# Kernel optimization log

Hardware: AMD Instinct MI355X
Metric: run time of the kernel (lower is better)

The kernel has to match this reference:

```python
import jax, jax.numpy as jnp
from jax import lax
import numpy as np

B, T, D, H, K = 16, 2048, 512, 512, 2

def setup_inputs() -> dict:
    key = jax.random.key(0)
    k1, k2, k3 = jax.random.split(key, 3)
    inputs = jax.random.normal(k1, (B, T, D), dtype=jnp.float32)
    conv_w = jax.random.normal(k2, (3 * H, D, K), dtype=jnp.float32) * (1.0 / np.sqrt(D * K))
    conv_b = jax.random.normal(k3, (3 * H,), dtype=jnp.float32) * 0.01
    return {"inputs": inputs, "conv_w": conv_w, "conv_b": conv_b}

def reference(inputs, conv_w, conv_b):
    # inputs: [B, T, D]; conv_w: [3H, D, K]; causal conv via left-pad K-1
    k = conv_w.shape[-1]
    h = conv_w.shape[0] // 3
    x = jnp.transpose(inputs, (0, 2, 1))                      # [B, D, T]
    x = jnp.pad(x, ((0, 0), (0, 0), (k - 1, 0)))              # left pad
    gates = lax.conv_general_dilated(
        x, conv_w, window_strides=(1,), padding='VALID',
        dimension_numbers=('NCH', 'OIH', 'NCH'))              # [B, 3H, T]
    gates = jnp.transpose(gates, (0, 2, 1)) + conv_b          # [B, T, 3H]
    Z, F, O = jnp.split(gates, 3, axis=2)
    Z = jnp.tanh(Z)
    F = jax.nn.sigmoid(F)
    O = jax.nn.sigmoid(O)

    # fo-pool: c_t = f_t * c_{t-1} + (1 - f_t) * z_t, c_{-1} = 0
    def step(c, zf):
        z, f = zf
        c_ = f * c + (1.0 - f) * z
        return c_, c_

    c0 = jnp.zeros((Z.shape[0], h), dtype=Z.dtype)
    _, C = lax.scan(step, c0, (jnp.swapaxes(Z, 0, 1), jnp.swapaxes(F, 0, 1)))
    C = jnp.swapaxes(C, 0, 1)                                 # [B, T, H]
    return C, O * C
```

## Files before the change

kernel.cpp:

```cpp
#include <hip/hip_runtime.h>


#define MTOT 32768
#define NTOT 1536
#define KTOT 1024
#define DCH  512
#define TLEN 2048
#define NB   16

#define SC 32
#define LC 64

typedef __bf16 bf16x8 __attribute__((ext_vector_type(8)));
typedef float  f32x4  __attribute__((ext_vector_type(4)));

__device__ __forceinline__ unsigned short f2bf(float x) {
    unsigned u = __float_as_uint(x);
    u += 0x7FFFu + ((u >> 16) & 1u);
    return (unsigned short)(u >> 16);
}
__device__ __forceinline__ float sigmoidf_(float x) {
    return 1.f / (1.f + __expf(-x));
}

__global__ __launch_bounds__(256) void make_A(const float* __restrict__ in,
                                              unsigned short* __restrict__ A) {
    size_t i = (size_t)blockIdx.x * 256 + threadIdx.x;
    size_t e = i * 8;
    size_t m = e >> 10;
    int    j = (int)(e & 1023);
    alignas(16) unsigned short h[8];
    if (((m & (TLEN - 1)) == 0) && (j < DCH)) {
#pragma unroll
        for (int r = 0; r < 8; ++r) h[r] = 0;
    } else {
        const float* src = in + ((long long)m - 1) * DCH + j;
        float4 a = *(const float4*)src;
        float4 b = *(const float4*)(src + 4);
        h[0] = f2bf(a.x); h[1] = f2bf(a.y); h[2] = f2bf(a.z); h[3] = f2bf(a.w);
        h[4] = f2bf(b.x); h[5] = f2bf(b.y); h[6] = f2bf(b.z); h[7] = f2bf(b.w);
    }
    *(int4*)(A + e) = *(const int4*)h;
}

__global__ __launch_bounds__(256) void make_B(const float* __restrict__ w,
                                              unsigned short* __restrict__ Bt) {
    int i = blockIdx.x * 256 + threadIdx.x;
    int o = i >> 9, d = i & 511;
    float w0 = w[(size_t)(o * 512 + d) * 2];
    float w1 = w[(size_t)(o * 512 + d) * 2 + 1];
    Bt[(size_t)o * 1024 + d]       = f2bf(w0);
    Bt[(size_t)o * 1024 + 512 + d] = f2bf(w1);
}

__global__ __launch_bounds__(256) void gemm_gates(const unsigned short* __restrict__ A,
                                                  const unsigned short* __restrict__ B,
                                                  const float* __restrict__ bias,
                                                  unsigned short* __restrict__ GT) {
    __shared__ int4 sA[512];
    __shared__ int4 sB[512];

    const int tid = threadIdx.x;
    const int bx  = blockIdx.x;
    const int xcd = bx & 7;
    const int i2  = bx >> 3;
    const int mT  = xcd * 32 + i2 / 12;
    const int nT  = i2 % 12;
    const int m0  = mT * 128, n0 = nT * 128;

    const int mloc = tid >> 2;
    const int qsw  = (tid & 3) ^ ((mloc >> 1) & 3);
    const unsigned short* ga0 = A + (size_t)(m0 + mloc) * 1024 + qsw * 8;
    const unsigned short* ga1 = A + (size_t)(m0 + 64 + mloc) * 1024 + qsw * 8;
    const unsigned short* gb0 = B + (size_t)(n0 + mloc) * 1024 + qsw * 8;
    const unsigned short* gb1 = B + (size_t)(n0 + 64 + mloc) * 1024 + qsw * 8;

    char* la0 = (char*)sA + tid * 16;
    char* la1 = (char*)sA + 4096 + tid * 16;
    char* lb0 = (char*)sB + tid * 16;
    char* lb1 = (char*)sB + 4096 + tid * 16;

    const int lane = tid & 63;
    const int wv   = tid >> 6;
    const int wm   = (wv & 1) * 64, wn = (wv >> 1) * 64;
    const int lr   = lane & 15, lq = lane >> 4;

    int sAidx[4], sBidx[4];
#pragma unroll
    for (int i = 0; i < 4; ++i) {
        int mi = wm + 16 * i + lr;
        sAidx[i] = mi * 4 + (lq ^ ((mi >> 1) & 3));
        int ni = wn + 16 * i + lr;
        sBidx[i] = ni * 4 + (lq ^ ((ni >> 1) & 3));
    }

    f32x4 acc[4][4] = {};

    for (int kt = 0; kt < KTOT; kt += 32) {
        __builtin_amdgcn_global_load_lds(
            (__attribute__((address_space(1))) void*)(void*)ga0,
            (__attribute__((address_space(3))) void*)la0, 16, 0, 0);
        __builtin_amdgcn_global_load_lds(
            (__attribute__((address_space(1))) void*)(void*)ga1,
            (__attribute__((address_space(3))) void*)la1, 16, 0, 0);
        __builtin_amdgcn_global_load_lds(
            (__attribute__((address_space(1))) void*)(void*)gb0,
            (__attribute__((address_space(3))) void*)lb0, 16, 0, 0);
        __builtin_amdgcn_global_load_lds(
            (__attribute__((address_space(1))) void*)(void*)gb1,
            (__attribute__((address_space(3))) void*)lb1, 16, 0, 0);
        ga0 += 32; ga1 += 32; gb0 += 32; gb1 += 32;
        __syncthreads();

        bf16x8 af[4], bfr[4];
#pragma unroll
        for (int i = 0; i < 4; ++i) af[i]  = __builtin_bit_cast(bf16x8, sA[sAidx[i]]);
#pragma unroll
        for (int j = 0; j < 4; ++j) bfr[j] = __builtin_bit_cast(bf16x8, sB[sBidx[j]]);

#pragma unroll
        for (int i = 0; i < 4; ++i)
#pragma unroll
            for (int j = 0; j < 4; ++j)
                acc[i][j] = __builtin_amdgcn_mfma_f32_16x16x32_bf16(af[i], bfr[j],
                                                                    acc[i][j], 0, 0, 0);
        __syncthreads();
    }

#pragma unroll
    for (int j = 0; j < 4; ++j) {
        int gn = n0 + wn + 16 * j + lr;
        float bj = bias[gn];
#pragma unroll
        for (int i = 0; i < 4; ++i) {
            int rowb = m0 + wm + 16 * i + lq * 4;
            alignas(8) unsigned short pk[4];
#pragma unroll
            for (int r = 0; r < 4; ++r) pk[r] = f2bf(acc[i][j][r] + bj);
            *(int2*)(GT + (size_t)gn * MTOT + rowb) = *(const int2*)pk;
        }
    }
}

__global__ __launch_bounds__(256) void scan_agg(const unsigned short* __restrict__ GT,
                                                float* __restrict__ P,
                                                float* __restrict__ C) {
    int idx = blockIdx.x * 256 + threadIdx.x;
    int h = idx & 511, s = (idx >> 9) & 31, b = idx >> 14;
    const unsigned short* gz = GT + (size_t)h * MTOT + (size_t)b * TLEN + s * LC;
    const unsigned short* gf = gz + (size_t)DCH * MTOT;

    float p = 1.f, c = 0.f;
#pragma unroll 2
    for (int k = 0; k < LC; k += 8) {
        bf16x8 zv = *(const bf16x8*)(gz + k);
        bf16x8 fv = *(const bf16x8*)(gf + k);
#pragma unroll
        for (int r = 0; r < 8; ++r) {
            float f = sigmoidf_((float)fv[r]);
            float z = 2.f * sigmoidf_(2.f * (float)zv[r]) - 1.f;
            c = f * c + (1.f - f) * z;
            p *= f;
        }
    }
    P[idx] = p;
    C[idx] = c;
}

__global__ __launch_bounds__(256) void scan_chunks(const float* __restrict__ P,
                                                   const float* __restrict__ C,
                                                   float* __restrict__ I) {
    int j = blockIdx.x * 256 + threadIdx.x;
    int b = j >> 9, h = j & 511;
    size_t base = (size_t)b * (SC * DCH) + h;
    float cc = 0.f;
#pragma unroll
    for (int s = 0; s < SC; ++s) {
        size_t o = base + (size_t)s * DCH;
        I[o] = cc;
        cc = P[o] * cc + C[o];
    }
}

__global__ __launch_bounds__(256) void scan_apply(const unsigned short* __restrict__ GT,
                                                  const float* __restrict__ I,
                                                  float* __restrict__ out) {
    int idx = blockIdx.x * 256 + threadIdx.x;
    int h = idx & 511, s = (idx >> 9) & 31, b = idx >> 14;
    const unsigned short* gz = GT + (size_t)h * MTOT + (size_t)b * TLEN + s * LC;
    const unsigned short* gf = gz + (size_t)DCH * MTOT;
    const unsigned short* go = gf + (size_t)DCH * MTOT;

    const size_t BTH = (size_t)NB * TLEN * DCH;
    float* oC  = out + ((size_t)b * TLEN + s * LC) * DCH + h;
    float* oOC = oC + BTH;

    float c = I[idx];
#pragma unroll 2
    for (int k = 0; k < LC; k += 8) {
        bf16x8 zv = *(const bf16x8*)(gz + k);
        bf16x8 fv = *(const bf16x8*)(gf + k);
        bf16x8 ov = *(const bf16x8*)(go + k);
#pragma unroll
        for (int r = 0; r < 8; ++r) {
            float f = sigmoidf_((float)fv[r]);
            float z = 2.f * sigmoidf_(2.f * (float)zv[r]) - 1.f;
            float o = sigmoidf_((float)ov[r]);
            c = f * c + (1.f - f) * z;
            oC[(size_t)(k + r) * DCH]  = c;
            oOC[(size_t)(k + r) * DCH] = o * c;
        }
    }
}

extern "C" void kernel_launch(void* const* d_in, const int* in_sizes, int n_in,
                              void* d_out, int out_size, void* d_ws, size_t ws_size,
                              hipStream_t stream) {
    const float* in   = (const float*)d_in[0];
    const float* w    = (const float*)d_in[1];
    const float* bias = (const float*)d_in[2];
    float* out = (float*)d_out;

    unsigned short* Abf = (unsigned short*)d_ws;
    unsigned short* Bbf = Abf + (size_t)MTOT * 1024;
    unsigned short* GT  = Bbf + (size_t)NTOT * 1024;

    float* P = (float*)d_ws;
    float* C = P + (size_t)NB * SC * DCH;
    float* I = C + (size_t)NB * SC * DCH;

    make_A<<<dim3(16384), dim3(256), 0, stream>>>(in, Abf);
    make_B<<<dim3(3072),  dim3(256), 0, stream>>>(w, Bbf);
    gemm_gates<<<dim3(3072), dim3(256), 0, stream>>>(Abf, Bbf, bias, GT);
    scan_agg<<<dim3(1024), dim3(256), 0, stream>>>(GT, P, C);
    scan_chunks<<<dim3(32), dim3(256), 0, stream>>>(P, C, I);
    scan_apply<<<dim3(1024), dim3(256), 0, stream>>>(GT, I, out);
}
```

Baseline: 427.1 us.

## Replace im2col buffer with padded input and vectorize scan kernels

Replaces the duplicated K=2 im2col A matrix with a single left-padded bf16 copy of the input. The GEMM reads each row's 1024-wide K slice as two consecutive padded rows, which halves the conversion kernel's writes and the workspace footprint. scan_agg now issues all of its gate loads up front. scan_apply handles two channels per thread with float2 output stores and batched register loads. The trade-off is higher register pressure and half as many blocks in scan_apply.

Measured after the change: 469.3 us. 9.9% more time.

```diff
diff --git a/kernel.cpp b/kernel.cpp
--- a/kernel.cpp
+++ b/kernel.cpp
@@ -23,24 +23,26 @@
     return 1.f / (1.f + __expf(-x));
 }
 
-__global__ __launch_bounds__(256) void make_A(const float* __restrict__ in,
-                                              unsigned short* __restrict__ A) {
-    size_t i = (size_t)blockIdx.x * 256 + threadIdx.x;
-    size_t e = i * 8;
-    size_t m = e >> 10;
-    int    j = (int)(e & 1023);
-    alignas(16) unsigned short h[8];
-    if (((m & (TLEN - 1)) == 0) && (j < DCH)) {
-#pragma unroll
-        for (int r = 0; r < 8; ++r) h[r] = 0;
+__global__ __launch_bounds__(256) void make_X(const float* __restrict__ in,
+                                              unsigned short* __restrict__ X) {
+    int rloc = threadIdx.x >> 6;
+    int c8   = (threadIdx.x & 63) << 3;
+    int row  = blockIdx.x * 4 + rloc;
+    int b    = blockIdx.y;
+    if (row >= 2049) return;
+    unsigned short* dst = X + ((size_t)b * 2049 + row) * 512 + c8;
+    alignas(16) unsigned short hh[8];
+    if (row == 0) {
+#pragma unroll
+        for (int r = 0; r < 8; ++r) hh[r] = 0;
     } else {
-        const float* src = in + ((long long)m - 1) * DCH + j;
+        const float* src = in + ((size_t)b * 2048 + row - 1) * 512 + c8;
         float4 a = *(const float4*)src;
-        float4 b = *(const float4*)(src + 4);
-        h[0] = f2bf(a.x); h[1] = f2bf(a.y); h[2] = f2bf(a.z); h[3] = f2bf(a.w);
-        h[4] = f2bf(b.x); h[5] = f2bf(b.y); h[6] = f2bf(b.z); h[7] = f2bf(b.w);
-    }
-    *(int4*)(A + e) = *(const int4*)h;
+        float4 v = *(const float4*)(src + 4);
+        hh[0] = f2bf(a.x); hh[1] = f2bf(a.y); hh[2] = f2bf(a.z); hh[3] = f2bf(a.w);
+        hh[4] = f2bf(v.x); hh[5] = f2bf(v.y); hh[6] = f2bf(v.z); hh[7] = f2bf(v.w);
+    }
+    *(int4*)dst = *(const int4*)hh;
 }
 
 __global__ __launch_bounds__(256) void make_B(const float* __restrict__ w,
@@ -53,7 +55,7 @@
     Bt[(size_t)o * 1024 + 512 + d] = f2bf(w1);
 }
 
-__global__ __launch_bounds__(256) void gemm_gates(const unsigned short* __restrict__ A,
+__global__ __launch_bounds__(256) void gemm_gates(const unsigned short* __restrict__ X,
                                                   const unsigned short* __restrict__ B,
                                                   const float* __restrict__ bias,
                                                   unsigned short* __restrict__ GT) {
@@ -67,11 +69,14 @@
     const int mT  = xcd * 32 + i2 / 12;
     const int nT  = i2 % 12;
     const int m0  = mT * 128, n0 = nT * 128;
+    const int b0  = m0 >> 11;
+    const int t0  = m0 & 2047;
 
     const int mloc = tid >> 2;
     const int qsw  = (tid & 3) ^ ((mloc >> 1) & 3);
-    const unsigned short* ga0 = A + (size_t)(m0 + mloc) * 1024 + qsw * 8;
-    const unsigned short* ga1 = A + (size_t)(m0 + 64 + mloc) * 1024 + qsw * 8;
+    const unsigned short* ga0 =
+        X + ((size_t)b0 * 2049 + t0 + mloc) * 512 + qsw * 8;
+    const unsigned short* ga1 = ga0 + (size_t)64 * 512;
     const unsigned short* gb0 = B + (size_t)(n0 + mloc) * 1024 + qsw * 8;
     const unsigned short* gb1 = B + (size_t)(n0 + 64 + mloc) * 1024 + qsw * 8;
 
@@ -147,14 +152,20 @@
                                                 float* __restrict__ C) {
     int idx = blockIdx.x * 256 + threadIdx.x;
     int h = idx & 511, s = (idx >> 9) & 31, b = idx >> 14;
-    const unsigned short* gz = GT + (size_t)h * MTOT + (size_t)b * TLEN + s * LC;
+    const unsigned short* gz = GT + (size_t)h * MTOT + (size_t)b * TLEN + (size_t)s * LC;
     const unsigned short* gf = gz + (size_t)DCH * MTOT;
 
+    int4 rz[8], rf[8];
+#pragma unroll
+    for (int q = 0; q < 8; ++q) rz[q] = *(const int4*)(gz + 8 * q);
+#pragma unroll
+    for (int q = 0; q < 8; ++q) rf[q] = *(const int4*)(gf + 8 * q);
+
     float p = 1.f, c = 0.f;
-#pragma unroll 2
-    for (int k = 0; k < LC; k += 8) {
-        bf16x8 zv = *(const bf16x8*)(gz + k);
-        bf16x8 fv = *(const bf16x8*)(gf + k);
+#pragma unroll
+    for (int q = 0; q < 8; ++q) {
+        bf16x8 zv = __builtin_bit_cast(bf16x8, rz[q]);
+        bf16x8 fv = __builtin_bit_cast(bf16x8, rf[q]);
 #pragma unroll
         for (int r = 0; r < 8; ++r) {
             float f = sigmoidf_((float)fv[r]);
@@ -185,30 +196,67 @@
 __global__ __launch_bounds__(256) void scan_apply(const unsigned short* __restrict__ GT,
                                                   const float* __restrict__ I,
                                                   float* __restrict__ out) {
-    int idx = blockIdx.x * 256 + threadIdx.x;
-    int h = idx & 511, s = (idx >> 9) & 31, b = idx >> 14;
-    const unsigned short* gz = GT + (size_t)h * MTOT + (size_t)b * TLEN + s * LC;
-    const unsigned short* gf = gz + (size_t)DCH * MTOT;
-    const unsigned short* go = gf + (size_t)DCH * MTOT;
+    const int tid = threadIdx.x;
+    const int s = blockIdx.x & 31;
+    const int b = blockIdx.x >> 5;
+    const int h = tid << 1;
+    const size_t mb = (size_t)b * TLEN + (size_t)s * LC;
+
+    const unsigned short* gz0 = GT + (size_t)h * MTOT + mb;
+    const unsigned short* gz1 = gz0 + MTOT;
+    const unsigned short* gf0 = gz0 + (size_t)DCH * MTOT;
+    const unsigned short* gf1 = gf0 + MTOT;
+    const unsigned short* go0 = gz0 + (size_t)(2 * DCH) * MTOT;
+    const unsigned short* go1 = go0 + MTOT;
 
     const size_t BTH = (size_t)NB * TLEN * DCH;
-    float* oC  = out + ((size_t)b * TLEN + s * LC) * DCH + h;
+    float* oC  = out + mb * DCH + h;
     float* oOC = oC + BTH;
 
-    float c = I[idx];
-#pragma unroll 2
-    for (int k = 0; k < LC; k += 8) {
-        bf16x8 zv = *(const bf16x8*)(gz + k);
-        bf16x8 fv = *(const bf16x8*)(gf + k);
-        bf16x8 ov = *(const bf16x8*)(go + k);
-#pragma unroll
-        for (int r = 0; r < 8; ++r) {
-            float f = sigmoidf_((float)fv[r]);
-            float z = 2.f * sigmoidf_(2.f * (float)zv[r]) - 1.f;
-            float o = sigmoidf_((float)ov[r]);
-            c = f * c + (1.f - f) * z;
-            oC[(size_t)(k + r) * DCH]  = c;
-            oOC[(size_t)(k + r) * DCH] = o * c;
+    size_t ib = (size_t)b * (SC * DCH) + (size_t)s * DCH + h;
+    float c0 = I[ib], c1 = I[ib + 1];
+
+#pragma unroll
+    for (int half = 0; half < 2; ++half) {
+        const int k0 = half * 32;
+        int4 rz0[4], rz1[4], rf0[4], rf1[4], ro0[4], ro1[4];
+#pragma unroll
+        for (int q = 0; q < 4; ++q) rz0[q] = *(const int4*)(gz0 + k0 + 8 * q);
+#pragma unroll
+        for (int q = 0; q < 4; ++q) rz1[q] = *(const int4*)(gz1 + k0 + 8 * q);
+#pragma unroll
+        for (int q = 0; q < 4; ++q) rf0[q] = *(const int4*)(gf0 + k0 + 8 * q);
+#pragma unroll
+        for (int q = 0; q < 4; ++q) rf1[q] = *(const int4*)(gf1 + k0 + 8 * q);
+#pragma unroll
+        for (int q = 0; q < 4; ++q) ro0[q] = *(const int4*)(go0 + k0 + 8 * q);
+#pragma unroll
+        for (int q = 0; q < 4; ++q) ro1[q] = *(const int4*)(go1 + k0 + 8 * q);
+
+#pragma unroll
+        for (int q = 0; q < 4; ++q) {
+            bf16x8 zv0 = __builtin_bit_cast(bf16x8, rz0[q]);
+            bf16x8 zv1 = __builtin_bit_cast(bf16x8, rz1[q]);
+            bf16x8 fv0 = __builtin_bit_cast(bf16x8, rf0[q]);
+            bf16x8 fv1 = __builtin_bit_cast(bf16x8, rf1[q]);
+            bf16x8 ov0 = __builtin_bit_cast(bf16x8, ro0[q]);
+            bf16x8 ov1 = __builtin_bit_cast(bf16x8, ro1[q]);
+#pragma unroll
+            for (int r = 0; r < 8; ++r) {
+                float f0 = sigmoidf_((float)fv0[r]);
+                float f1 = sigmoidf_((float)fv1[r]);
+                float z0 = 2.f * sigmoidf_(2.f * (float)zv0[r]) - 1.f;
+                float z1 = 2.f * sigmoidf_(2.f * (float)zv1[r]) - 1.f;
+                float o0 = sigmoidf_((float)ov0[r]);
+                float o1 = sigmoidf_((float)ov1[r]);
+                c0 = f0 * c0 + (1.f - f0) * z0;
+                c1 = f1 * c1 + (1.f - f1) * z1;
+                size_t off = (size_t)(k0 + q * 8 + r) * DCH;
+                float2 cc; cc.x = c0; cc.y = c1;
+                *(float2*)(oC + off) = cc;
+                float2 oc; oc.x = o0 * c0; oc.y = o1 * c1;
+                *(float2*)(oOC + off) = oc;
+            }
         }
     }
 }
@@ -221,18 +269,18 @@
     const float* bias = (const float*)d_in[2];
     float* out = (float*)d_out;
 
-    unsigned short* Abf = (unsigned short*)d_ws;
-    unsigned short* Bbf = Abf + (size_t)MTOT * 1024;
-    unsigned short* GT  = Bbf + (size_t)NTOT * 1024;
+    unsigned short* Xpad = (unsigned short*)d_ws;
+    unsigned short* Bbf  = Xpad + (size_t)NB * 2049 * 512;
+    unsigned short* GT   = Bbf + (size_t)NTOT * 1024;
 
     float* P = (float*)d_ws;
     float* C = P + (size_t)NB * SC * DCH;
     float* I = C + (size_t)NB * SC * DCH;
 
-    make_A<<<dim3(16384), dim3(256), 0, stream>>>(in, Abf);
-    make_B<<<dim3(3072),  dim3(256), 0, stream>>>(w, Bbf);
-    gemm_gates<<<dim3(3072), dim3(256), 0, stream>>>(Abf, Bbf, bias, GT);
+    make_X<<<dim3(513, 16), dim3(256), 0, stream>>>(in, Xpad);
+    make_B<<<dim3(3072), dim3(256), 0, stream>>>(w, Bbf);
+    gemm_gates<<<dim3(3072), dim3(256), 0, stream>>>(Xpad, Bbf, bias, GT);
     scan_agg<<<dim3(1024), dim3(256), 0, stream>>>(GT, P, C);
     scan_chunks<<<dim3(32), dim3(256), 0, stream>>>(P, C, I);
-    scan_apply<<<dim3(1024), dim3(256), 0, stream>>>(GT, I, out);
-}
+    scan_apply<<<dim3(512), dim3(256), 0, stream>>>(GT, I, out);
+}
```
